# Kernel optimization log

Hardware: AMD Instinct MI355X
Metric: run time of the kernel (lower is better)

## Reference

```python
import jax, jax.numpy as jnp
import numpy as np

B, T, NH, HD, VD = 2, 2048, 16, 128, 256
KD = NH * HD            # 2048
VDIM = NH * VD          # 4096
EPS = 1e-12


def _l2norm(x):
    # torch.nn.functional.normalize: x / max(||x||_2, eps)
    n = jnp.sqrt(jnp.sum(x * x, axis=-1, keepdims=True))
    return x / jnp.maximum(n, EPS)


def setup_inputs() -> dict:
    key = jax.random.key(0)
    k1, k2 = jax.random.split(key)
    x = jax.random.normal(k1, (B, T, KD), dtype=jnp.float32)
    W = jax.random.normal(k2, (2 * KD + VDIM + 2 * NH, KD), dtype=jnp.float32) * 0.02
    state = jnp.zeros((B, NH, VD, HD), dtype=jnp.float32)
    return {"x": x, "W": W, "state": state}


def reference(x, W, state):
    # shared projection (no bias)
    proj = jnp.einsum('btd,od->bto', x, W)  # [B,T,2*KD+VDIM+2*NH]
    q = proj[..., :KD].reshape(B, T, NH, HD)
    k = proj[..., KD:2 * KD].reshape(B, T, NH, HD)
    v = proj[..., 2 * KD:2 * KD + VDIM].reshape(B, T, NH, VD)
    g = jax.nn.sigmoid(proj[..., 2 * KD + VDIM:2 * KD + VDIM + NH])      # [B,T,NH] decay gate
    beta = jax.nn.sigmoid(proj[..., 2 * KD + VDIM + NH:])                # [B,T,NH]
    q = _l2norm(q)
    k = _l2norm(k)

    # time-major for scan
    qs = jnp.moveaxis(q, 1, 0)      # [T,B,NH,HD]
    ks = jnp.moveaxis(k, 1, 0)
    vs = jnp.moveaxis(v, 1, 0)      # [T,B,NH,VD]
    gs = jnp.moveaxis(g, 1, 0)      # [T,B,NH]
    bs = jnp.moveaxis(beta, 1, 0)

    def step(S, inp):
        # gated delta rule: S_t = g*S - g*b*(S k) k^T + b*v k^T ; o_t = S_t q
        q_t, k_t, v_t, g_t, b_t = inp
        Sk = jnp.einsum('bnvh,bnh->bnv', S, k_t)                         # [B,NH,VD]
        delta = b_t[..., None] * (v_t - g_t[..., None] * Sk)             # [B,NH,VD]
        S_new = g_t[..., None, None] * S + delta[..., None] * k_t[:, :, None, :]
        o = jnp.einsum('bnvh,bnh->bnv', S_new, q_t)                      # [B,NH,VD]
        return S_new, o

    _, out = jax.lax.scan(step, state, (qs, ks, vs, gs, bs))
    return jnp.moveaxis(out, 0, 1)  # [B,T,NH,VD]
```

## Files before the change

kernel.cpp:

```cpp
#include <hip/hip_runtime.h>
#include <hip/hip_bf16.h>
#include <cstdint>


typedef __attribute__((ext_vector_type(8))) short short8;
typedef __attribute__((ext_vector_type(4))) float f32x4;
typedef unsigned short u16;

using as1_void = __attribute__((address_space(1))) void;
using as3_void = __attribute__((address_space(3))) void;

__device__ __forceinline__ void gll16(const void* g, void* l) {
  __builtin_amdgcn_global_load_lds((const as1_void*)g, (as3_void*)l, 16, 0, 0);
}

__device__ __forceinline__ u16 bf16_rne(float f) {
  union { float f; uint32_t u; } x; x.f = f;
  uint32_t u = x.u;
  return (u16)((u + 0x7fffu + ((u >> 16) & 1u)) >> 16);
}
__device__ __forceinline__ float bf2f(u16 v) {
  union { uint32_t u; float f; } x; x.u = (uint32_t)v << 16;
  return x.f;
}

#define LGKM_BAR() do {                                      \
    asm volatile("s_waitcnt lgkmcnt(0)" ::: "memory");       \
    __builtin_amdgcn_s_barrier();                            \
    __builtin_amdgcn_sched_barrier(0);                       \
  } while (0)

#define SCHED_FENCE() __builtin_amdgcn_sched_barrier(0)
#define HW_BAR() __builtin_amdgcn_s_barrier()
#define LGKM0() asm volatile("s_waitcnt lgkmcnt(0)" ::: "memory")
#define VMCNT(n) asm volatile("s_waitcnt vmcnt(" #n ")" ::: "memory")

__global__ __launch_bounds__(256) void cvt_f32_bf16(const float* __restrict__ in,
                                                    u16* __restrict__ out, int n4) {
  int i = blockIdx.x * 256 + threadIdx.x;
  if (i < n4) {
    float4 v = ((const float4*)in)[i];
    ushort4 o;
    o.x = bf16_rne(v.x); o.y = bf16_rne(v.y);
    o.z = bf16_rne(v.z); o.w = bf16_rne(v.w);
    ((ushort4*)out)[i] = o;
  }
}

__global__ __launch_bounds__(256, 1) void gate_kernel(const float* __restrict__ x,
                                                      const float* __restrict__ W,
                                                      float* __restrict__ gbuf,
                                                      u16* __restrict__ xb) {
  const int w = threadIdx.x >> 6, lane = threadIdx.x & 63;
  const int r0 = (blockIdx.x * 4 + w) * 4;
  const float* xr = x + (size_t)r0 * 2048 + lane * 32;
  float4 xv[4][8];
#pragma unroll
  for (int i = 0; i < 4; ++i)
#pragma unroll
    for (int j = 0; j < 8; ++j)
      xv[i][j] = ((const float4*)(xr + (size_t)i * 2048))[j];
#pragma unroll
  for (int i = 0; i < 4; ++i) {
    u16* xrow = xb + (size_t)(r0 + i) * 2048 + lane * 32;
#pragma unroll
    for (int j = 0; j < 8; ++j) {
      ushort4 o;
      o.x = bf16_rne(xv[i][j].x); o.y = bf16_rne(xv[i][j].y);
      o.z = bf16_rne(xv[i][j].z); o.w = bf16_rne(xv[i][j].w);
      ((ushort4*)xrow)[j] = o;
    }
  }
  for (int col = 0; col < 32; ++col) {
    const float* wp = W + (size_t)(8192 + col) * 2048 + lane * 32;
    float4 wv[8];
#pragma unroll
    for (int j = 0; j < 8; ++j) wv[j] = ((const float4*)wp)[j];
    float d[4] = {0.f, 0.f, 0.f, 0.f};
#pragma unroll
    for (int i = 0; i < 4; ++i)
#pragma unroll
      for (int j = 0; j < 8; ++j)
        d[i] += xv[i][j].x * wv[j].x + xv[i][j].y * wv[j].y +
                xv[i][j].z * wv[j].z + xv[i][j].w * wv[j].w;
#pragma unroll
    for (int i = 0; i < 4; ++i) {
      d[i] += __shfl_xor(d[i], 1);  d[i] += __shfl_xor(d[i], 2);
      d[i] += __shfl_xor(d[i], 4);  d[i] += __shfl_xor(d[i], 8);
      d[i] += __shfl_xor(d[i], 16); d[i] += __shfl_xor(d[i], 32);
    }
    if (lane == 0) {
#pragma unroll
      for (int i = 0; i < 4; ++i) {
        int rv = r0 + i, b = rv >> 11, t = rv & 2047;
        float s = 1.f / (1.f + __expf(-d[i]));
        gbuf[((size_t)(b * 16 + (col & 15)) * 2048 + t) * 2 + (col >> 4)] = s;
      }
    }
  }
}

__global__ __launch_bounds__(512, 2) void gemm_bf16_btn(const u16* __restrict__ A,
                                                        const u16* __restrict__ B,
                                                        u16* __restrict__ qb,
                                                        u16* __restrict__ kb,
                                                        u16* __restrict__ vb) {
  __shared__ __align__(16) u16 As[2][16384];
  __shared__ __align__(16) u16 Bs[2][16384];
  __shared__ float nrm[2][4][128];

  const int tid = threadIdx.x;
  const int wid = tid >> 6, lane = tid & 63;
  const int lr = lane & 15, lk = lane >> 4;
  const int wr = wid >> 2, wc = wid & 3;

  const int wg = ((blockIdx.x & 7) << 6) | (blockIdx.x >> 3);
  const int bm = wg >> 5, bn = wg & 31;

  const int e8s = (tid & 7) ^ (((tid >> 3) & 1) << 2) ^ (((tid >> 5) & 1) << 1);
  const int srow = tid >> 3;
  const u16* Agb = A + (size_t)(bm * 256 + srow) * 2048 + e8s * 8;
  const u16* Bgb = B + (size_t)(bn * 256 + srow) * 2048 + e8s * 8;

  const int kkx = lr & 1;
  const int lkp = lk ^ (((lr >> 2) & 1) << 1);
  const int aOff0 = (wr * 128 + lr) * 64 + kkx * 32 + lkp * 8;
  const int aOff1 = (wr * 128 + lr) * 64 + (1 ^ kkx) * 32 + lkp * 8;
  const int bOff0 = (wc * 64 + lr) * 64 + kkx * 32 + lkp * 8;
  const int bOff1 = (wc * 64 + lr) * 64 + (1 ^ kkx) * 32 + lkp * 8;

  auto stageA = [&](int bf, int kt, int h) {
    const u16* s = Agb + (size_t)(h * 128) * 2048 + kt * 64;
    u16* d = &As[bf][h * 8192 + wid * 512];
    gll16(s, d);
    gll16(s + (size_t)64 * 2048, d + 4096);
  };
  auto stageB = [&](int bf, int kt, int h) {
    const u16* s = Bgb + (size_t)(h * 128) * 2048 + kt * 64;
    u16* d = &Bs[bf][h * 8192 + wid * 512];
    gll16(s, d);
    gll16(s + (size_t)64 * 2048, d + 4096);
  };

  f32x4 acc[8][4] = {};

  stageA(0, 0, 0); stageA(0, 0, 1);
  stageB(0, 0, 0); stageB(0, 0, 1);
  stageA(1, 1, 0); stageA(1, 1, 1);
  stageB(1, 1, 0);
  VMCNT(6);
  SCHED_FENCE();
  HW_BAR();

#define QUAD(M0, N0)                                                          \
  do {                                                                        \
    __builtin_amdgcn_s_setprio(1);                                            \
    _Pragma("unroll")                                                         \
    for (int m_ = 0; m_ < 4; ++m_)                                            \
      _Pragma("unroll")                                                       \
      for (int n_ = 0; n_ < 2; ++n_) {                                        \
        acc[M0 + m_][N0 + n_] = __builtin_amdgcn_mfma_f32_16x16x32_bf16(      \
            a[M0 + m_][0], b[N0 + n_][0], acc[M0 + m_][N0 + n_], 0, 0, 0);    \
        acc[M0 + m_][N0 + n_] = __builtin_amdgcn_mfma_f32_16x16x32_bf16(      \
            a[M0 + m_][1], b[N0 + n_][1], acc[M0 + m_][N0 + n_], 0, 0, 0);    \
      }                                                                       \
    __builtin_amdgcn_s_setprio(0);                                            \
  } while (0)

  for (int kt = 0; kt < 32; ++kt) {
    const int bf = kt & 1;
    const u16* pA0 = &As[bf][aOff0];
    const u16* pA1 = &As[bf][aOff1];
    const u16* pB0 = &Bs[bf][bOff0];
    const u16* pB1 = &Bs[bf][bOff1];
    short8 a[8][2], b[4][2];

#pragma unroll
    for (int m = 0; m < 8; ++m) {
      a[m][0] = *(const short8*)(pA0 + m * 1024);
      a[m][1] = *(const short8*)(pA1 + m * 1024);
    }
#pragma unroll
    for (int n = 0; n < 2; ++n) {
      b[n][0] = *(const short8*)(pB0 + n * 1024);
      b[n][1] = *(const short8*)(pB1 + n * 1024);
    }
    SCHED_FENCE();
    if (kt < 31) stageB((kt + 1) & 1, kt + 1, 1);
    SCHED_FENCE(); HW_BAR(); LGKM0(); SCHED_FENCE();
    QUAD(0, 0);
    SCHED_FENCE(); HW_BAR();

#pragma unroll
    for (int n = 2; n < 4; ++n) {
      b[n][0] = *(const short8*)(pB0 + n * 1024);
      b[n][1] = *(const short8*)(pB1 + n * 1024);
    }
    SCHED_FENCE();
    if (kt < 30) stageA(bf, kt + 2, 0);
    SCHED_FENCE(); HW_BAR(); LGKM0(); SCHED_FENCE();
    QUAD(0, 2);
    SCHED_FENCE(); HW_BAR();

    if (kt < 30) stageA(bf, kt + 2, 1);
    SCHED_FENCE(); HW_BAR(); SCHED_FENCE();
    QUAD(4, 0);
    SCHED_FENCE(); HW_BAR();

    if (kt < 30) stageB(bf, kt + 2, 0);
    SCHED_FENCE(); HW_BAR(); SCHED_FENCE();
    QUAD(4, 2);
    SCHED_FENCE();
    if (kt < 30) { VMCNT(6); } else if (kt == 30) { VMCNT(0); }
    SCHED_FENCE(); HW_BAR();
  }
#undef QUAD

  if (bn < 16) {
#pragma unroll
    for (int m = 0; m < 8; ++m)
#pragma unroll
      for (int r = 0; r < 4; ++r) {
        float s = 0.f;
#pragma unroll
        for (int nn = 0; nn < 4; ++nn) {
          float v = bf2f(bf16_rne(acc[m][nn][r]));
          s += v * v;
        }
        s += __shfl_xor(s, 1); s += __shfl_xor(s, 2);
        s += __shfl_xor(s, 4); s += __shfl_xor(s, 8);
        if (lr == 0) nrm[wr][wc][m * 16 + lk * 4 + r] = s;
      }
    __syncthreads();
#pragma unroll
    for (int m = 0; m < 8; ++m)
#pragma unroll
      for (int r = 0; r < 4; ++r) {
        int rloc = m * 16 + lk * 4 + r;
        float ss = nrm[wr][wc][rloc] + nrm[wr][wc ^ 1][rloc];
        float sc = 1.f / fmaxf(sqrtf(ss), 1e-12f);
        int row = bm * 256 + wr * 128 + rloc;
        int bb = row >> 11, tt = row & 2047;
#pragma unroll
        for (int nn = 0; nn < 4; ++nn) {
          int col = bn * 256 + wc * 64 + nn * 16 + lr;
          int head = (col >> 7) & 15;
          int h = col & 127;
          u16 val = bf16_rne(bf2f(bf16_rne(acc[m][nn][r])) * sc);
          u16* dst = (col < 2048) ? qb : kb;
          dst[((size_t)(bb * 16 + head) * 2048 + tt) * 128 + h] = val;
        }
      }
  } else {
#pragma unroll
    for (int m = 0; m < 8; ++m)
#pragma unroll
      for (int nn = 0; nn < 4; ++nn)
#pragma unroll
        for (int r = 0; r < 4; ++r) {
          int row = bm * 256 + wr * 128 + m * 16 + lk * 4 + r;
          int col = bn * 256 + wc * 64 + nn * 16 + lr;
          int bb = row >> 11, tt = row & 2047;
          u16 val = bf16_rne(acc[m][nn][r]);
          int vh = col - 4096;
          vb[((size_t)(bb * 16 + (vh >> 8)) * 2048 + tt) * 256 + (vh & 255)] = val;
        }
  }
}

__global__ __launch_bounds__(256) void chunk_prep(const u16* __restrict__ qb,
                                                  const u16* __restrict__ kb,
                                                  const float* __restrict__ gbuf,
                                                  float* __restrict__ gp,
                                                  u16* __restrict__ Tm,
                                                  u16* __restrict__ Pm) {
  __shared__ u16 Kc[64 * 128];
  __shared__ u16 Qc[64 * 128];
  __shared__ u16 Nn[64 * 64];
  __shared__ u16 NT[64 * 64];
  __shared__ u16 Tt[64 * 64];
  __shared__ u16 TTt[64 * 64];
  __shared__ float gl[256];
  __shared__ float Lw[64];
  __shared__ float bw[64];

  const int bid = blockIdx.x;
  const int seq = bid >> 5, c = bid & 31;
  const int t0 = c * 64;
  const int tid = threadIdx.x;
  const int w = tid >> 6, lane = tid & 63;
  const int lr = lane & 15, lk = lane >> 4;
  const int lr7 = lr & 7;

  {
    const int rowo = lane >> 4;
    const int c8e = (lane & 15) ^ rowo;
    const int c8o = (lane & 15) ^ (4 | rowo);
    if (w == 0) {
      const u16* se = kb + ((size_t)seq * 2048 + t0 + rowo) * 128 + c8e * 8;
      const u16* so = kb + ((size_t)seq * 2048 + t0 + rowo) * 128 + c8o * 8;
#pragma unroll
      for (int i = 0; i < 16; ++i)
        gll16(((i & 1) ? so : se) + (size_t)i * 512, &Kc[i * 512]);
    } else if (w == 1) {
      const u16* se = qb + ((size_t)seq * 2048 + t0 + rowo) * 128 + c8e * 8;
      const u16* so = qb + ((size_t)seq * 2048 + t0 + rowo) * 128 + c8o * 8;
#pragma unroll
      for (int i = 0; i < 16; ++i)
        gll16(((i & 1) ? so : se) + (size_t)i * 512, &Qc[i * 512]);
    } else if (w == 2) {
      gll16(gbuf + (size_t)seq * 4096 + c * 128 + lane * 4, &gl[0]);
    }
  }
  __syncthreads();

  if (w == 0) {
    float g = gl[2 * lane], b = gl[2 * lane + 1];
    float lg = __logf(g);
#pragma unroll
    for (int d = 1; d < 64; d <<= 1) {
      float y = __shfl_up(lg, d);
      if (lane >= d) lg += y;
    }
    Lw[lane] = lg;
    bw[lane] = b;
    float G = __expf(lg);
    float L63 = __shfl(lg, 63);
    float wgt = __expf(L63 - lg);
    float* gpo = gp + ((size_t)seq * 32 + c) * 256;
    gpo[lane] = b;
    gpo[64 + lane] = b * G;
    gpo[128 + lane] = G;
    gpo[192 + lane] = wgt;
  }
  __syncthreads();

  f32x4 kkacc[4] = {}, qkacc[4] = {};
#pragma unroll
  for (int ct = 0; ct < 4; ++ct)
#pragma unroll
    for (int k0 = 0; k0 < 4; ++k0) {
      const int sl = ((k0 * 4 + lk) ^ lr7) << 3;
      short8 bfr = *(const short8*)&Kc[(ct * 16 + lr) * 128 + sl];
      short8 afk = *(const short8*)&Kc[(w * 16 + lr) * 128 + sl];
      short8 afq = *(const short8*)&Qc[(w * 16 + lr) * 128 + sl];
      kkacc[ct] = __builtin_amdgcn_mfma_f32_16x16x32_bf16(afk, bfr, kkacc[ct], 0, 0, 0);
      qkacc[ct] = __builtin_amdgcn_mfma_f32_16x16x32_bf16(afq, bfr, qkacc[ct], 0, 0, 0);
    }
  u16* Pout = Pm + ((size_t)seq * 32 + c) * 4096;
#pragma unroll
  for (int ct = 0; ct < 4; ++ct)
#pragma unroll
    for (int r = 0; r < 4; ++r) {
      int s = w * 16 + lk * 4 + r;
      int cc = ct * 16 + lr;
      int iA = s * 64 + ((((ct * 2 + (lr >> 3)) ^ (s & 7)) << 3)) + lr7;
      int iB = cc * 64 + ((((s >> 3) ^ lr7) << 3)) + (s & 7);
      u16 nv = 0;
      if (cc < s)
        nv = bf16_rne(-(bw[s] * __expf(Lw[s] - Lw[cc]) * kkacc[ct][r]));
      Nn[iA] = nv;
      NT[iB] = nv;
      u16 tv = (cc == s) ? (u16)0x3F80 : nv;
      Tt[iA] = tv;
      TTt[iB] = tv;
      u16 pv = 0;
      if (cc <= s)
        pv = bf16_rne(__expf(Lw[s] - Lw[cc]) * qkacc[ct][r]);
      Pout[s * 64 + cc] = pv;
    }
  __syncthreads();

  u16* Tout = Tm + ((size_t)seq * 32 + c) * 4096;
#pragma unroll 1
  for (int j = 0; j < 5; ++j) {
    f32x4 acc2[4] = {};
#pragma unroll
    for (int ct = 0; ct < 4; ++ct)
#pragma unroll
      for (int k0 = 0; k0 < 2; ++k0) {
        const int sl = ((k0 * 4 + lk) ^ lr7) << 3;
        short8 af = *(const short8*)&Nn[(w * 16 + lr) * 64 + sl];
        short8 bfr = *(const short8*)&NT[(ct * 16 + lr) * 64 + sl];
        acc2[ct] = __builtin_amdgcn_mfma_f32_16x16x32_bf16(af, bfr, acc2[ct], 0, 0, 0);
      }
    __syncthreads();
#pragma unroll
    for (int ct = 0; ct < 4; ++ct)
#pragma unroll
      for (int r = 0; r < 4; ++r) {
        int s = w * 16 + lk * 4 + r, cc = ct * 16 + lr;
        int iA = s * 64 + ((((ct * 2 + (lr >> 3)) ^ (s & 7)) << 3)) + lr7;
        int iB = cc * 64 + ((((s >> 3) ^ lr7) << 3)) + (s & 7);
        u16 v = bf16_rne(acc2[ct][r]);
        Nn[iA] = v;
        NT[iB] = v;
      }
    __syncthreads();
    f32x4 acc3[4];
#pragma unroll
    for (int ct = 0; ct < 4; ++ct)
#pragma unroll
      for (int r = 0; r < 4; ++r) {
        int a = w * 16 + lk * 4 + r;
        acc3[ct][r] = bf2f(Tt[a * 64 + ((((ct * 2 + (lr >> 3)) ^ (a & 7)) << 3)) + lr7]);
      }
#pragma unroll
    for (int ct = 0; ct < 4; ++ct)
#pragma unroll
      for (int k0 = 0; k0 < 2; ++k0) {
        const int sl = ((k0 * 4 + lk) ^ lr7) << 3;
        short8 af = *(const short8*)&Nn[(w * 16 + lr) * 64 + sl];
        short8 bfr = *(const short8*)&TTt[(ct * 16 + lr) * 64 + sl];
        acc3[ct] = __builtin_amdgcn_mfma_f32_16x16x32_bf16(af, bfr, acc3[ct], 0, 0, 0);
      }
    __syncthreads();
    if (j < 4) {
#pragma unroll
      for (int ct = 0; ct < 4; ++ct)
#pragma unroll
        for (int r = 0; r < 4; ++r) {
          int s = w * 16 + lk * 4 + r, cc = ct * 16 + lr;
          int iA = s * 64 + ((((ct * 2 + (lr >> 3)) ^ (s & 7)) << 3)) + lr7;
          int iB = cc * 64 + ((((s >> 3) ^ lr7) << 3)) + (s & 7);
          u16 v = bf16_rne(acc3[ct][r]);
          Tt[iA] = v;
          TTt[iB] = v;
        }
      __syncthreads();
    } else {
#pragma unroll
      for (int ct = 0; ct < 4; ++ct)
#pragma unroll
        for (int r = 0; r < 4; ++r) {
          int s = w * 16 + lk * 4 + r, cc = ct * 16 + lr;
          Tout[s * 64 + cc] = bf16_rne(acc3[ct][r]);
        }
    }
  }
}

__global__ __launch_bounds__(512) void chunk_scan(const u16* __restrict__ qb,
                                                  const u16* __restrict__ kb,
                                                  const u16* __restrict__ vb,
                                                  const float* __restrict__ gp,
                                                  const u16* __restrict__ Tm,
                                                  const u16* __restrict__ Pm,
                                                  const float* __restrict__ st0,
                                                  float* __restrict__ out) {
  __shared__ u16 Kc[2][64 * 128];
  __shared__ u16 Qc[2][64 * 128];
  __shared__ u16 Vc[2][64 * 32];
  __shared__ u16 Tc[2][64 * 64];
  __shared__ u16 Pc[2][64 * 64];
  __shared__ float gpl[2][256];
  __shared__ u16 KTw[128 * 64];
  __shared__ u16 Sb[32 * 128];
  __shared__ u16 RT[32 * 64];
  __shared__ u16 UT[32 * 64];

  const int bid = blockIdx.x;
  const int shard = bid >> 5, seq = bid & 31;
  const int vs0 = shard * 32;
  const int b = seq >> 4, n = seq & 15;
  const int tid = threadIdx.x;
  const int w = tid >> 6, lane = tid & 63;
  const int lr = lane & 15, lk = lane >> 4;
  const int lr7 = lr & 7;
  const int w3 = w & 3;
  const int vt = w & 1, hgb = (w >> 1) * 2;

  const u16* kbase = kb + (size_t)seq * 2048 * 128;
  const u16* qbase = qb + (size_t)seq * 2048 * 128;
  const u16* vbase = vb + (size_t)seq * 2048 * 256 + vs0;
  const float* gpbase = gp + (size_t)seq * 32 * 256;
  const u16* Tbase = Tm + (size_t)seq * 32 * 4096;
  const u16* Pbase = Pm + (size_t)seq * 32 * 4096;

  const int rowo = lane >> 4;
  const int c8e = (lane & 15) ^ rowo;
  const int c8o = (lane & 15) ^ (4 | rowo);
  const int tp8 = (lane & 7) ^ (lane >> 3);
  const int vc8 = (lane & 3) ^ (lane >> 4);

  auto stage = [&](int sb, int c) {
    const int t0 = c * 64;
    if (w == 0 || w == 4) {
      const int i0 = (w == 0) ? 0 : 8;
      const u16* se = kbase + (size_t)(t0 + rowo) * 128 + c8e * 8;
      const u16* so = kbase + (size_t)(t0 + rowo) * 128 + c8o * 8;
#pragma unroll
      for (int i = 0; i < 8; ++i) {
        const int ii = i0 + i;
        gll16(((ii & 1) ? so : se) + (size_t)ii * 512, &Kc[sb][ii * 512]);
      }
    } else if (w == 1 || w == 5) {
      const int i0 = (w == 1) ? 0 : 8;
      const u16* se = qbase + (size_t)(t0 + rowo) * 128 + c8e * 8;
      const u16* so = qbase + (size_t)(t0 + rowo) * 128 + c8o * 8;
#pragma unroll
      for (int i = 0; i < 8; ++i) {
        const int ii = i0 + i;
        gll16(((ii & 1) ? so : se) + (size_t)ii * 512, &Qc[sb][ii * 512]);
      }
    } else if (w == 2) {
      const u16* srcT = Tbase + (size_t)c * 4096 + (lane >> 3) * 64 + tp8 * 8;
#pragma unroll
      for (int i = 0; i < 8; ++i) gll16(srcT + (size_t)i * 512, &Tc[sb][i * 512]);
    } else if (w == 6) {
      const u16* srcP = Pbase + (size_t)c * 4096 + (lane >> 3) * 64 + tp8 * 8;
#pragma unroll
      for (int i = 0; i < 8; ++i) gll16(srcP + (size_t)i * 512, &Pc[sb][i * 512]);
    } else if (w == 3) {
      const u16* src = vbase + (size_t)(t0 + (lane >> 2)) * 256 + vc8 * 8;
#pragma unroll
      for (int i = 0; i < 4; ++i) gll16(src + (size_t)i * 4096, &Vc[sb][i * 512]);
    } else {
      gll16(gpbase + (size_t)c * 256 + lane * 4, &gpl[sb][0]);
    }
  };

  f32x4 s_acc[2];
  {
    const float* s0p = st0 + ((size_t)seq * 256 + vs0) * 128;
#pragma unroll
    for (int ht = 0; ht < 2; ++ht)
#pragma unroll
      for (int r = 0; r < 4; ++r)
        s_acc[ht][r] = s0p[(size_t)(vt * 16 + lk * 4 + r) * 128 + (hgb + ht) * 16 + lr];
  }
  stage(0, 0);
  __syncthreads();

  for (int c = 0; c < 32; ++c) {
    const int buf = c & 1;
    const int t0 = c * 64;

    stage(buf ^ 1, (c < 31) ? c + 1 : 31);
#pragma unroll
    for (int ht = 0; ht < 2; ++ht)
#pragma unroll
      for (int r = 0; r < 4; ++r) {
        int row = vt * 16 + lk * 4 + r;
        int c8 = (hgb + ht) * 2 + (lr >> 3);
        Sb[row * 128 + ((c8 ^ (row & 7)) << 3) + lr7] = bf16_rne(s_acc[ht][r]);
      }
    {
      const int s = tid >> 3;
      const int cb = (tid & 7) * 2;
      const float ws = gpl[buf][192 + s];
      short8 kv0 = *(const short8*)&Kc[buf][s * 128 + ((cb ^ (s & 7)) << 3)];
      short8 kv1 = *(const short8*)&Kc[buf][s * 128 + (((cb + 1) ^ (s & 7)) << 3)];
#pragma unroll
      for (int j = 0; j < 8; ++j) {
        int row = cb * 8 + j;
        KTw[row * 64 + (((s >> 3) ^ (j & 7)) << 3) + (s & 7)] =
            bf16_rne(ws * bf2f((u16)kv0[j]));
      }
#pragma unroll
      for (int j = 0; j < 8; ++j) {
        int row = cb * 8 + 8 + j;
        KTw[row * 64 + (((s >> 3) ^ (j & 7)) << 3) + (s & 7)] =
            bf16_rne(ws * bf2f((u16)kv1[j]));
      }
    }
    LGKM_BAR();

    f32x4 mm_acc[2] = {};
    if (w < 4) {
#pragma unroll
      for (int ct = 0; ct < 2; ++ct)
#pragma unroll
        for (int k0 = 0; k0 < 4; ++k0) {
          const int sl = ((k0 * 4 + lk) ^ lr7) << 3;
          short8 bfr = *(const short8*)&Sb[(ct * 16 + lr) * 128 + sl];
          short8 afk = *(const short8*)&Kc[buf][(w3 * 16 + lr) * 128 + sl];
          mm_acc[ct] = __builtin_amdgcn_mfma_f32_16x16x32_bf16(afk, bfr, mm_acc[ct], 0, 0, 0);
        }
#pragma unroll
      for (int ct = 0; ct < 2; ++ct)
#pragma unroll
        for (int r = 0; r < 4; ++r) {
          int t = w3 * 16 + lk * 4 + r;
          int j2 = ct * 16 + lr;
          float bt = gpl[buf][t], bG = gpl[buf][64 + t];
          float vv = bf2f(Vc[buf][t * 32 + ((((ct * 2 + (lr >> 3)) ^ lk)) << 3) + lr7]);
          float rv = bt * vv - bG * mm_acc[ct][r];
          RT[j2 * 64 + (((t >> 3) ^ lr7) << 3) + (t & 7)] = bf16_rne(rv);
        }
    } else {
#pragma unroll
      for (int ct = 0; ct < 2; ++ct)
#pragma unroll
        for (int k0 = 0; k0 < 4; ++k0) {
          const int sl = ((k0 * 4 + lk) ^ lr7) << 3;
          short8 bfr = *(const short8*)&Sb[(ct * 16 + lr) * 128 + sl];
          short8 afq = *(const short8*)&Qc[buf][(w3 * 16 + lr) * 128 + sl];
          mm_acc[ct] = __builtin_amdgcn_mfma_f32_16x16x32_bf16(afq, bfr, mm_acc[ct], 0, 0, 0);
        }
    }
    LGKM_BAR();

    if (w < 4) {
      f32x4 u_acc[2] = {};
#pragma unroll
      for (int ct = 0; ct < 2; ++ct)
#pragma unroll
        for (int k0 = 0; k0 < 2; ++k0) {
          const int sl = ((k0 * 4 + lk) ^ lr7) << 3;
          short8 af = *(const short8*)&Tc[buf][(w3 * 16 + lr) * 64 + sl];
          short8 bfr = *(const short8*)&RT[(ct * 16 + lr) * 64 + sl];
          u_acc[ct] = __builtin_amdgcn_mfma_f32_16x16x32_bf16(af, bfr, u_acc[ct], 0, 0, 0);
        }
#pragma unroll
      for (int ct = 0; ct < 2; ++ct)
#pragma unroll
        for (int r = 0; r < 4; ++r) {
          int s2 = w3 * 16 + lk * 4 + r;
          int j2 = ct * 16 + lr;
          UT[j2 * 64 + (((s2 >> 3) ^ lr7) << 3) + (s2 & 7)] = bf16_rne(u_acc[ct][r]);
        }
    }
    LGKM_BAR();

    {
      const float Gc = gpl[buf][128 + 63];
#pragma unroll
      for (int ht = 0; ht < 2; ++ht) {
        s_acc[ht][0] *= Gc; s_acc[ht][1] *= Gc;
        s_acc[ht][2] *= Gc; s_acc[ht][3] *= Gc;
      }
#pragma unroll
      for (int ht = 0; ht < 2; ++ht)
#pragma unroll
        for (int k0 = 0; k0 < 2; ++k0) {
          const int sl = ((k0 * 4 + lk) ^ lr7) << 3;
          short8 af = *(const short8*)&UT[(vt * 16 + lr) * 64 + sl];
          short8 bfr = *(const short8*)&KTw[((hgb + ht) * 16 + lr) * 64 + sl];
          s_acc[ht] = __builtin_amdgcn_mfma_f32_16x16x32_bf16(af, bfr, s_acc[ht], 0, 0, 0);
        }
    }
    if (w >= 4) {
      f32x4 o_acc[2];
#pragma unroll
      for (int ct = 0; ct < 2; ++ct)
#pragma unroll
        for (int r = 0; r < 4; ++r) {
          int t = w3 * 16 + lk * 4 + r;
          o_acc[ct][r] = gpl[buf][128 + t] * mm_acc[ct][r];
        }
#pragma unroll
      for (int ct = 0; ct < 2; ++ct)
#pragma unroll
        for (int k0 = 0; k0 < 2; ++k0) {
          const int sl = ((k0 * 4 + lk) ^ lr7) << 3;
          short8 af = *(const short8*)&Pc[buf][(w3 * 16 + lr) * 64 + sl];
          short8 bfr = *(const short8*)&UT[(ct * 16 + lr) * 64 + sl];
          o_acc[ct] = __builtin_amdgcn_mfma_f32_16x16x32_bf16(af, bfr, o_acc[ct], 0, 0, 0);
        }
#pragma unroll
      for (int ct = 0; ct < 2; ++ct)
#pragma unroll
        for (int r = 0; r < 4; ++r) {
          int t = w3 * 16 + lk * 4 + r;
          int j2 = ct * 16 + lr;
          out[(((size_t)b * 2048 + t0 + t) * 16 + n) * 256 + vs0 + j2] = o_acc[ct][r];
        }
    }
    __syncthreads();
  }
}

extern "C" void kernel_launch(void* const* d_in, const int* in_sizes, int n_in,
                              void* d_out, int out_size, void* d_ws, size_t ws_size,
                              hipStream_t stream) {
  const float* x = (const float*)d_in[0];
  const float* W = (const float*)d_in[1];
  const float* st0 = (const float*)d_in[2];
  float* out = (float*)d_out;
  char* ws = (char*)d_ws;

  u16* xb   = (u16*)ws;
  u16* Wb   = (u16*)(ws + 16777216);
  u16* qb   = (u16*)(ws + 50331648);
  u16* kb   = (u16*)(ws + 67108864);
  u16* vb   = (u16*)(ws + 83886080);
  float* gb = (float*)(ws + 117440512);
  float* gp = (float*)(ws + 123731968);
  u16* Tm   = (u16*)(ws + 125829120);
  u16* Pm   = (u16*)(ws + 134217728);

  cvt_f32_bf16<<<16384, 256, 0, stream>>>(W, Wb, 4194304);
  gate_kernel<<<256, 256, 0, stream>>>(x, W, gb, xb);
  gemm_bf16_btn<<<512, 512, 0, stream>>>(xb, Wb, qb, kb, vb);
  chunk_prep<<<1024, 256, 0, stream>>>(qb, kb, gb, gp, Tm, Pm);
  chunk_scan<<<256, 512, 0, stream>>>(qb, kb, vb, gp, Tm, Pm, st0, out);
}
```

Baseline: 353.2 us.

## Double chunk_scan block to 1024 threads, one MFMA tile per wave

Launches the chunk-scan kernel with 16 waves instead of 8 and repartitions the work. Each wave now owns one 16x16 output tile per matmul stage instead of two, and the staging loads and the K transpose are spread over twice as many waves. This shortens the serial per-chunk critical path of the sequential scan, which runs on only 256 blocks. In exchange it adds more waves to each block-wide barrier and limits occupancy to one block per CU.

Result: slower. 380.4 us (+7.7%).

```diff
diff --git a/kernel.cpp b/kernel.cpp
--- a/kernel.cpp
+++ b/kernel.cpp
@@ -440,14 +440,14 @@
   }
 }
 
-__global__ __launch_bounds__(512) void chunk_scan(const u16* __restrict__ qb,
-                                                  const u16* __restrict__ kb,
-                                                  const u16* __restrict__ vb,
-                                                  const float* __restrict__ gp,
-                                                  const u16* __restrict__ Tm,
-                                                  const u16* __restrict__ Pm,
-                                                  const float* __restrict__ st0,
-                                                  float* __restrict__ out) {
+__global__ __launch_bounds__(1024, 1) void chunk_scan(const u16* __restrict__ qb,
+                                                      const u16* __restrict__ kb,
+                                                      const u16* __restrict__ vb,
+                                                      const float* __restrict__ gp,
+                                                      const u16* __restrict__ Tm,
+                                                      const u16* __restrict__ Pm,
+                                                      const float* __restrict__ st0,
+                                                      float* __restrict__ out) {
   __shared__ u16 Kc[2][64 * 128];
   __shared__ u16 Qc[2][64 * 128];
   __shared__ u16 Vc[2][64 * 32];
@@ -467,8 +467,9 @@
   const int w = tid >> 6, lane = tid & 63;
   const int lr = lane & 15, lk = lane >> 4;
   const int lr7 = lr & 7;
-  const int w3 = w & 3;
-  const int vt = w & 1, hgb = (w >> 1) * 2;
+  const int wm = w & 7;
+  const int rt = wm >> 1, ctf = wm & 1;
+  const int vt = w & 1, hg = w >> 1;
 
   const u16* kbase = kb + (size_t)seq * 2048 * 128;
   const u16* qbase = qb + (size_t)seq * 2048 * 128;
@@ -485,49 +486,57 @@
 
   auto stage = [&](int sb, int c) {
     const int t0 = c * 64;
-    if (w == 0 || w == 4) {
-      const int i0 = (w == 0) ? 0 : 8;
+    const int cls = w & 3;
+    if (cls == 0) {
+      const int i0 = (w >> 2) * 4;
       const u16* se = kbase + (size_t)(t0 + rowo) * 128 + c8e * 8;
       const u16* so = kbase + (size_t)(t0 + rowo) * 128 + c8o * 8;
 #pragma unroll
-      for (int i = 0; i < 8; ++i) {
+      for (int i = 0; i < 4; ++i) {
         const int ii = i0 + i;
         gll16(((ii & 1) ? so : se) + (size_t)ii * 512, &Kc[sb][ii * 512]);
       }
-    } else if (w == 1 || w == 5) {
-      const int i0 = (w == 1) ? 0 : 8;
+    } else if (cls == 1) {
+      const int i0 = (w >> 2) * 4;
       const u16* se = qbase + (size_t)(t0 + rowo) * 128 + c8e * 8;
       const u16* so = qbase + (size_t)(t0 + rowo) * 128 + c8o * 8;
 #pragma unroll
-      for (int i = 0; i < 8; ++i) {
+      for (int i = 0; i < 4; ++i) {
         const int ii = i0 + i;
         gll16(((ii & 1) ? so : se) + (size_t)ii * 512, &Qc[sb][ii * 512]);
       }
-    } else if (w == 2) {
-      const u16* srcT = Tbase + (size_t)c * 4096 + (lane >> 3) * 64 + tp8 * 8;
-#pragma unroll
-      for (int i = 0; i < 8; ++i) gll16(srcT + (size_t)i * 512, &Tc[sb][i * 512]);
-    } else if (w == 6) {
-      const u16* srcP = Pbase + (size_t)c * 4096 + (lane >> 3) * 64 + tp8 * 8;
-#pragma unroll
-      for (int i = 0; i < 8; ++i) gll16(srcP + (size_t)i * 512, &Pc[sb][i * 512]);
-    } else if (w == 3) {
-      const u16* src = vbase + (size_t)(t0 + (lane >> 2)) * 256 + vc8 * 8;
-#pragma unroll
-      for (int i = 0; i < 4; ++i) gll16(src + (size_t)i * 4096, &Vc[sb][i * 512]);
+    } else if (cls == 2) {
+      const int i0 = (w >> 3) * 4;
+      if ((w & 4) == 0) {
+        const u16* srcT = Tbase + (size_t)c * 4096 + (lane >> 3) * 64 + tp8 * 8;
+#pragma unroll
+        for (int i = 0; i < 4; ++i)
+          gll16(srcT + (size_t)(i0 + i) * 512, &Tc[sb][(i0 + i) * 512]);
+      } else {
+        const u16* srcP = Pbase + (size_t)c * 4096 + (lane >> 3) * 64 + tp8 * 8;
+#pragma unroll
+        for (int i = 0; i < 4; ++i)
+          gll16(srcP + (size_t)(i0 + i) * 512, &Pc[sb][(i0 + i) * 512]);
+      }
     } else {
-      gll16(gpbase + (size_t)c * 256 + lane * 4, &gpl[sb][0]);
+      if (w == 3 || w == 11) {
+        const int i0 = (w == 3) ? 0 : 2;
+        const u16* src = vbase + (size_t)(t0 + (lane >> 2)) * 256 + vc8 * 8;
+#pragma unroll
+        for (int i = 0; i < 2; ++i)
+          gll16(src + (size_t)(i0 + i) * 4096, &Vc[sb][(i0 + i) * 512]);
+      } else if (w == 7) {
+        gll16(gpbase + (size_t)c * 256 + lane * 4, &gpl[sb][0]);
+      }
     }
   };
 
-  f32x4 s_acc[2];
+  f32x4 s_acc;
   {
     const float* s0p = st0 + ((size_t)seq * 256 + vs0) * 128;
 #pragma unroll
-    for (int ht = 0; ht < 2; ++ht)
-#pragma unroll
-      for (int r = 0; r < 4; ++r)
-        s_acc[ht][r] = s0p[(size_t)(vt * 16 + lk * 4 + r) * 128 + (hgb + ht) * 16 + lr];
+    for (int r = 0; r < 4; ++r)
+      s_acc[r] = s0p[(size_t)(vt * 16 + lk * 4 + r) * 128 + hg * 16 + lr];
   }
   stage(0, 0);
   __syncthreads();
@@ -538,134 +547,103 @@
 
     stage(buf ^ 1, (c < 31) ? c + 1 : 31);
 #pragma unroll
-    for (int ht = 0; ht < 2; ++ht)
-#pragma unroll
-      for (int r = 0; r < 4; ++r) {
-        int row = vt * 16 + lk * 4 + r;
-        int c8 = (hgb + ht) * 2 + (lr >> 3);
-        Sb[row * 128 + ((c8 ^ (row & 7)) << 3) + lr7] = bf16_rne(s_acc[ht][r]);
-      }
+    for (int r = 0; r < 4; ++r) {
+      int row = vt * 16 + lk * 4 + r;
+      int c8 = hg * 2 + (lr >> 3);
+      Sb[row * 128 + ((c8 ^ (row & 7)) << 3) + lr7] = bf16_rne(s_acc[r]);
+    }
     {
-      const int s = tid >> 3;
-      const int cb = (tid & 7) * 2;
+      const int s = tid >> 4;
+      const int cb = tid & 15;
       const float ws = gpl[buf][192 + s];
-      short8 kv0 = *(const short8*)&Kc[buf][s * 128 + ((cb ^ (s & 7)) << 3)];
-      short8 kv1 = *(const short8*)&Kc[buf][s * 128 + (((cb + 1) ^ (s & 7)) << 3)];
+      short8 kv = *(const short8*)&Kc[buf][s * 128 + ((cb ^ (s & 7)) << 3)];
 #pragma unroll
       for (int j = 0; j < 8; ++j) {
         int row = cb * 8 + j;
-        KTw[row * 64 + (((s >> 3) ^ (j & 7)) << 3) + (s & 7)] =
-            bf16_rne(ws * bf2f((u16)kv0[j]));
-      }
-#pragma unroll
-      for (int j = 0; j < 8; ++j) {
-        int row = cb * 8 + 8 + j;
-        KTw[row * 64 + (((s >> 3) ^ (j & 7)) << 3) + (s & 7)] =
-            bf16_rne(ws * bf2f((u16)kv1[j]));
+        KTw[row * 64 + (((s >> 3) ^ j) << 3) + (s & 7)] =
+            bf16_rne(ws * bf2f((u16)kv[j]));
       }
     }
     LGKM_BAR();
 
-    f32x4 mm_acc[2] = {};
-    if (w < 4) {
-#pragma unroll
-      for (int ct = 0; ct < 2; ++ct)
-#pragma unroll
-        for (int k0 = 0; k0 < 4; ++k0) {
-          const int sl = ((k0 * 4 + lk) ^ lr7) << 3;
-          short8 bfr = *(const short8*)&Sb[(ct * 16 + lr) * 128 + sl];
-          short8 afk = *(const short8*)&Kc[buf][(w3 * 16 + lr) * 128 + sl];
-          mm_acc[ct] = __builtin_amdgcn_mfma_f32_16x16x32_bf16(afk, bfr, mm_acc[ct], 0, 0, 0);
-        }
-#pragma unroll
-      for (int ct = 0; ct < 2; ++ct)
-#pragma unroll
-        for (int r = 0; r < 4; ++r) {
-          int t = w3 * 16 + lk * 4 + r;
-          int j2 = ct * 16 + lr;
-          float bt = gpl[buf][t], bG = gpl[buf][64 + t];
-          float vv = bf2f(Vc[buf][t * 32 + ((((ct * 2 + (lr >> 3)) ^ lk)) << 3) + lr7]);
-          float rv = bt * vv - bG * mm_acc[ct][r];
-          RT[j2 * 64 + (((t >> 3) ^ lr7) << 3) + (t & 7)] = bf16_rne(rv);
-        }
+    f32x4 mm_acc = {};
+    if (w < 8) {
+#pragma unroll
+      for (int k0 = 0; k0 < 4; ++k0) {
+        const int sl = ((k0 * 4 + lk) ^ lr7) << 3;
+        short8 bfr = *(const short8*)&Sb[(ctf * 16 + lr) * 128 + sl];
+        short8 afk = *(const short8*)&Kc[buf][(rt * 16 + lr) * 128 + sl];
+        mm_acc = __builtin_amdgcn_mfma_f32_16x16x32_bf16(afk, bfr, mm_acc, 0, 0, 0);
+      }
+#pragma unroll
+      for (int r = 0; r < 4; ++r) {
+        int t = rt * 16 + lk * 4 + r;
+        int j2 = ctf * 16 + lr;
+        float bt = gpl[buf][t], bG = gpl[buf][64 + t];
+        float vv = bf2f(Vc[buf][t * 32 + ((((ctf * 2 + (lr >> 3)) ^ lk)) << 3) + lr7]);
+        float rv = bt * vv - bG * mm_acc[r];
+        RT[j2 * 64 + (((t >> 3) ^ lr7) << 3) + (t & 7)] = bf16_rne(rv);
+      }
     } else {
 #pragma unroll
-      for (int ct = 0; ct < 2; ++ct)
-#pragma unroll
-        for (int k0 = 0; k0 < 4; ++k0) {
-          const int sl = ((k0 * 4 + lk) ^ lr7) << 3;
-          short8 bfr = *(const short8*)&Sb[(ct * 16 + lr) * 128 + sl];
-          short8 afq = *(const short8*)&Qc[buf][(w3 * 16 + lr) * 128 + sl];
-          mm_acc[ct] = __builtin_amdgcn_mfma_f32_16x16x32_bf16(afq, bfr, mm_acc[ct], 0, 0, 0);
-        }
+      for (int k0 = 0; k0 < 4; ++k0) {
+        const int sl = ((k0 * 4 + lk) ^ lr7) << 3;
+        short8 bfr = *(const short8*)&Sb[(ctf * 16 + lr) * 128 + sl];
+        short8 afq = *(const short8*)&Qc[buf][(rt * 16 + lr) * 128 + sl];
+        mm_acc = __builtin_amdgcn_mfma_f32_16x16x32_bf16(afq, bfr, mm_acc, 0, 0, 0);
+      }
     }
     LGKM_BAR();
 
-    if (w < 4) {
-      f32x4 u_acc[2] = {};
-#pragma unroll
-      for (int ct = 0; ct < 2; ++ct)
-#pragma unroll
-        for (int k0 = 0; k0 < 2; ++k0) {
-          const int sl = ((k0 * 4 + lk) ^ lr7) << 3;
-          short8 af = *(const short8*)&Tc[buf][(w3 * 16 + lr) * 64 + sl];
-          short8 bfr = *(const short8*)&RT[(ct * 16 + lr) * 64 + sl];
-          u_acc[ct] = __builtin_amdgcn_mfma_f32_16x16x32_bf16(af, bfr, u_acc[ct], 0, 0, 0);
-        }
-#pragma unroll
-      for (int ct = 0; ct < 2; ++ct)
-#pragma unroll
-        for (int r = 0; r < 4; ++r) {
-          int s2 = w3 * 16 + lk * 4 + r;
-          int j2 = ct * 16 + lr;
-          UT[j2 * 64 + (((s2 >> 3) ^ lr7) << 3) + (s2 & 7)] = bf16_rne(u_acc[ct][r]);
-        }
+    if (w < 8) {
+      f32x4 u_acc = {};
+#pragma unroll
+      for (int k0 = 0; k0 < 2; ++k0) {
+        const int sl = ((k0 * 4 + lk) ^ lr7) << 3;
+        short8 af = *(const short8*)&Tc[buf][(rt * 16 + lr) * 64 + sl];
+        short8 bfr = *(const short8*)&RT[(ctf * 16 + lr) * 64 + sl];
+        u_acc = __builtin_amdgcn_mfma_f32_16x16x32_bf16(af, bfr, u_acc, 0, 0, 0);
+      }
+#pragma unroll
+      for (int r = 0; r < 4; ++r) {
+        int s2 = rt * 16 + lk * 4 + r;
+        int j2 = ctf * 16 + lr;
+        UT[j2 * 64 + (((s2 >> 3) ^ lr7) << 3) + (s2 & 7)] = bf16_rne(u_acc[r]);
+      }
     }
     LGKM_BAR();
 
     {
       const float Gc = gpl[buf][128 + 63];
-#pragma unroll
-      for (int ht = 0; ht < 2; ++ht) {
-        s_acc[ht][0] *= Gc; s_acc[ht][1] *= Gc;
-        s_acc[ht][2] *= Gc; s_acc[ht][3] *= Gc;
-      }
-#pragma unroll
-      for (int ht = 0; ht < 2; ++ht)
-#pragma unroll
-        for (int k0 = 0; k0 < 2; ++k0) {
-          const int sl = ((k0 * 4 + lk) ^ lr7) << 3;
-          short8 af = *(const short8*)&UT[(vt * 16 + lr) * 64 + sl];
-          short8 bfr = *(const short8*)&KTw[((hgb + ht) * 16 + lr) * 64 + sl];
-          s_acc[ht] = __builtin_amdgcn_mfma_f32_16x16x32_bf16(af, bfr, s_acc[ht], 0, 0, 0);
-        }
-    }
-    if (w >= 4) {
-      f32x4 o_acc[2];
-#pragma unroll
-      for (int ct = 0; ct < 2; ++ct)
-#pragma unroll
-        for (int r = 0; r < 4; ++r) {
-          int t = w3 * 16 + lk * 4 + r;
-          o_acc[ct][r] = gpl[buf][128 + t] * mm_acc[ct][r];
-        }
-#pragma unroll
-      for (int ct = 0; ct < 2; ++ct)
-#pragma unroll
-        for (int k0 = 0; k0 < 2; ++k0) {
-          const int sl = ((k0 * 4 + lk) ^ lr7) << 3;
-          short8 af = *(const short8*)&Pc[buf][(w3 * 16 + lr) * 64 + sl];
-          short8 bfr = *(const short8*)&UT[(ct * 16 + lr) * 64 + sl];
-          o_acc[ct] = __builtin_amdgcn_mfma_f32_16x16x32_bf16(af, bfr, o_acc[ct], 0, 0, 0);
-        }
-#pragma unroll
-      for (int ct = 0; ct < 2; ++ct)
-#pragma unroll
-        for (int r = 0; r < 4; ++r) {
-          int t = w3 * 16 + lk * 4 + r;
-          int j2 = ct * 16 + lr;
-          out[(((size_t)b * 2048 + t0 + t) * 16 + n) * 256 + vs0 + j2] = o_acc[ct][r];
-        }
+      s_acc[0] *= Gc; s_acc[1] *= Gc; s_acc[2] *= Gc; s_acc[3] *= Gc;
+#pragma unroll
+      for (int k0 = 0; k0 < 2; ++k0) {
+        const int sl = ((k0 * 4 + lk) ^ lr7) << 3;
+        short8 af = *(const short8*)&UT[(vt * 16 + lr) * 64 + sl];
+        short8 bfr = *(const short8*)&KTw[(hg * 16 + lr) * 64 + sl];
+        s_acc = __builtin_amdgcn_mfma_f32_16x16x32_bf16(af, bfr, s_acc, 0, 0, 0);
+      }
+    }
+    if (w >= 8) {
+      f32x4 o_acc;
+#pragma unroll
+      for (int r = 0; r < 4; ++r) {
+        int t = rt * 16 + lk * 4 + r;
+        o_acc[r] = gpl[buf][128 + t] * mm_acc[r];
+      }
+#pragma unroll
+      for (int k0 = 0; k0 < 2; ++k0) {
+        const int sl = ((k0 * 4 + lk) ^ lr7) << 3;
+        short8 af = *(const short8*)&Pc[buf][(rt * 16 + lr) * 64 + sl];
+        short8 bfr = *(const short8*)&UT[(ctf * 16 + lr) * 64 + sl];
+        o_acc = __builtin_amdgcn_mfma_f32_16x16x32_bf16(af, bfr, o_acc, 0, 0, 0);
+      }
+#pragma unroll
+      for (int r = 0; r < 4; ++r) {
+        int t = rt * 16 + lk * 4 + r;
+        int j2 = ctf * 16 + lr;
+        out[(((size_t)b * 2048 + t0 + t) * 16 + n) * 256 + vs0 + j2] = o_acc[r];
+      }
     }
     __syncthreads();
   }
@@ -694,5 +672,5 @@
   gate_kernel<<<256, 256, 0, stream>>>(x, W, gb, xb);
   gemm_bf16_btn<<<512, 512, 0, stream>>>(xb, Wb, qb, kb, vb);
   chunk_prep<<<1024, 256, 0, stream>>>(qb, kb, gb, gp, Tm, Pm);
-  chunk_scan<<<256, 512, 0, stream>>>(qb, kb, vb, gp, Tm, Pm, st0, out);
-}
+  chunk_scan<<<256, 1024, 0, stream>>>(qb, kb, vb, gp, Tm, Pm, st0, out);
+}
```
